# Kernel optimization log

Hardware: AMD Instinct MI355X
Metric: run time of the kernel (lower is better)

Reference implementation:

```python
import jax, jax.numpy as jnp
import numpy as np

R = 8          # n attention heads / input capsules (config_spin['r'])
U2 = 1024      # 2 * d_lstm
DA = 512       # d_a
SC = 128       # n_seen_class
OA = 16        # output_atoms
NR = 3         # n_routing
B = 128
T = 256


def setup_inputs() -> dict:
    key = jax.random.key(0)
    k1, k2, k3, k4 = jax.random.split(key, 4)
    x = jax.random.normal(k1, (B, T, U2), jnp.float32)              # encoder output outp
    WS1 = jax.random.normal(k2, (R, DA, U2), jnp.float32) * 0.03    # r stacked Linear(2u->d_a) weights
    WS2 = jax.random.normal(k3, (R, U2, DA), jnp.float32) * 0.03    # r stacked Linear(d_a->2u) weights
    capsule_weights = jax.random.normal(k4, (R, U2, SC * OA), jnp.float32) * 0.03
    return {"x": x, "WS1": WS1, "WS2": WS2, "capsule_weights": capsule_weights}


def _squash(s):
    # s: [B, out_dim, atoms]; squash along atoms (dim=2 in torch)
    norm = jnp.linalg.norm(s, axis=2, keepdims=True)
    n2 = norm * norm
    return s / norm * (n2 / (1.0 + n2))


def reference(x, WS1, WS2, capsule_weights):
    # --- encoder_dim_att: r-head structured self-attention ---
    hbar = jax.nn.relu(jnp.einsum('btu,rau->brta', x, WS1))          # [B,r,T,d_a]
    scores = jnp.einsum('brta,rua->brtu', hbar, WS2)                 # [B,r,T,2u]
    alphas = jax.nn.softmax(scores, axis=2)                          # softmax over seq (torch dim=1)
    m = jnp.einsum('brtu,btu->bru', alphas, x)                       # sentence_embedding [B,r,2u]

    # --- votes: tiled multiply+sum == contraction over input_atoms ---
    votes = jnp.einsum('bru,ruo->bro', m, capsule_weights)           # [B,r,SC*OA]
    votes = votes.reshape(B, R, SC, OA)                              # [B,r,SC,OA]

    # --- dynamic routing ---
    logits0 = jnp.zeros((B, R, SC), x.dtype)

    def step(logits, _):
        route = jax.nn.softmax(logits, axis=2)                       # [B,r,SC]
        preact = jnp.einsum('brc,brco->bco', route, votes)           # [B,SC,OA]
        act = _squash(preact)                                        # [B,SC,OA]
        dist = jnp.einsum('brco,bco->brc', votes, act)               # agreement [B,r,SC]
        return logits + dist, act

    _, acts = jax.lax.scan(step, logits0, None, length=NR)
    activation = acts[-1]                                            # last-iteration activation
    return jnp.linalg.norm(activation, axis=-1)                      # class logits [B,SC]
```

## Files before the change

### kernel.cpp

```cpp
#include <hip/hip_runtime.h>


typedef __attribute__((ext_vector_type(8))) short bf16x8;
typedef __attribute__((ext_vector_type(8))) unsigned short u16x8;
typedef __attribute__((ext_vector_type(4))) float f32x4;

#define LDT 40

__device__ __forceinline__ unsigned short f2bf(float f) {
    unsigned u = __float_as_uint(f);
    u += 0x7FFF + ((u >> 16) & 1);
    return (unsigned short)(u >> 16);
}
__device__ __forceinline__ float bf2f(unsigned short h) {
    return __uint_as_float(((unsigned)h) << 16);
}

typedef __attribute__((address_space(1))) void gvoid;
typedef __attribute__((address_space(3))) void lvoid;
__device__ __forceinline__ void gll16(const unsigned short* g, unsigned short* l) {
    __builtin_amdgcn_global_load_lds((gvoid*)g, (lvoid*)l, 16, 0, 0);
}

__global__ __launch_bounds__(256) void k0_hi(const float* __restrict__ src,
                                             unsigned short* __restrict__ hi,
                                             int n4) {
    int i = blockIdx.x * 256 + threadIdx.x;
    if (i >= n4) return;
    float4 v = ((const float4*)src)[i];
    ushort4 h;
    h.x = f2bf(v.x); h.y = f2bf(v.y); h.z = f2bf(v.z); h.w = f2bf(v.w);
    ((ushort4*)hi)[i] = h;
}

__global__ __launch_bounds__(256) void k0_tsplit(const float* __restrict__ cw,
                                                 unsigned short* __restrict__ ch,
                                                 unsigned short* __restrict__ cl) {
    __shared__ unsigned short Th[64 * 68], Tl[64 * 68];
    const int tid = threadIdx.x;
    const int n0 = blockIdx.x * 64, k0 = blockIdx.y * 64, r = blockIdx.z;
    const float* src = cw + (size_t)r * 1024 * 2048;
#pragma unroll
    for (int p = 0; p < 4; p++) {
        const int kl = p * 16 + (tid >> 4);
        const int nl = (tid & 15) * 4;
        float4 v = *(const float4*)(src + (size_t)(k0 + kl) * 2048 + n0 + nl);
        float vv[4] = {v.x, v.y, v.z, v.w};
#pragma unroll
        for (int e = 0; e < 4; e++) {
            unsigned short h = f2bf(vv[e]);
            Th[(nl + e) * 68 + kl] = h;
            Tl[(nl + e) * 68 + kl] = f2bf(vv[e] - bf2f(h));
        }
    }
    __syncthreads();
    const int nl = tid >> 2, kl = (tid & 3) * 16;
    unsigned short* dh = ch + ((size_t)r * 2048 + n0 + nl) * 1024 + k0 + kl;
    unsigned short* dl = cl + ((size_t)r * 2048 + n0 + nl) * 1024 + k0 + kl;
    *(u16x8*)(dh)     = *(const u16x8*)&Th[nl * 68 + kl];
    *(u16x8*)(dh + 8) = *(const u16x8*)&Th[nl * 68 + kl + 8];
    *(u16x8*)(dl)     = *(const u16x8*)&Tl[nl * 68 + kl];
    *(u16x8*)(dl + 8) = *(const u16x8*)&Tl[nl * 68 + kl + 8];
}

__global__ __launch_bounds__(256) void k1_hbar_gll(
    const unsigned short* __restrict__ Xb,
    const unsigned short* __restrict__ Wh,
    unsigned short* __restrict__ Hh) {
    __shared__ __align__(16) unsigned short Ah[128 * 32];
    __shared__ __align__(16) unsigned short Bh[128 * 32];
    const int tid = threadIdx.x;
    const int m0 = blockIdx.x * 128, n0 = blockIdx.y * 128;
    const int wave = tid >> 6, lane = tid & 63;
    const int wm = (wave >> 1) * 64, wn = (wave & 1) * 64;
    const int lx = lane & 15, qd = lane >> 4;
    const int rl = lane >> 2, cl = (lane & 3) * 8;

    f32x4 acc[4][4];
#pragma unroll
    for (int i = 0; i < 4; i++)
#pragma unroll
        for (int j = 0; j < 4; j++) acc[i][j] = (f32x4){0.f, 0.f, 0.f, 0.f};

    const unsigned short* asrc = Xb + (size_t)(m0 + rl) * 1024 + cl;
    const unsigned short* bsrc = Wh + (size_t)(n0 + rl) * 1024 + cl;

    for (int k0 = 0; k0 < 1024; k0 += 32) {
#pragma unroll
        for (int s = 0; s < 2; s++) {
            const int c = wave * 2 + s;
            gll16(asrc + (size_t)c * 16 * 1024 + k0, &Ah[c * 512]);
            gll16(bsrc + (size_t)c * 16 * 1024 + k0, &Bh[c * 512]);
        }
        __syncthreads();
        bf16x8 fa[4], fb[4];
#pragma unroll
        for (int i = 0; i < 4; i++) {
            fa[i] = *(const bf16x8*)&Ah[(wm + 16 * i + lx) * 32 + 8 * qd];
            fb[i] = *(const bf16x8*)&Bh[(wn + 16 * i + lx) * 32 + 8 * qd];
        }
#pragma unroll
        for (int i = 0; i < 4; i++)
#pragma unroll
            for (int j = 0; j < 4; j++)
                acc[i][j] = __builtin_amdgcn_mfma_f32_16x16x32_bf16(fa[i], fb[j], acc[i][j], 0, 0, 0);
        __syncthreads();
    }

#pragma unroll
    for (int i = 0; i < 4; i++)
#pragma unroll
        for (int j = 0; j < 4; j++) {
            const int col = n0 + wn + 16 * j + lx;
#pragma unroll
            for (int p = 0; p < 4; p++) {
                const int row = m0 + wm + 16 * i + 4 * qd + p;
                Hh[(size_t)row * 512 + col] = f2bf(fmaxf(acc[i][j][p], 0.f));
            }
        }
}

template <int XBF>
__global__ __launch_bounds__(256) void k1_hbar_mfma(
    const void* __restrict__ Xv,
    const unsigned short* __restrict__ Wh,
    unsigned short* __restrict__ Hh) {
    __shared__ unsigned short Ah[128 * LDT];
    __shared__ unsigned short Bh[128 * LDT];
    const int tid = threadIdx.x;
    const int m0 = blockIdx.x * 128, n0 = blockIdx.y * 128;
    const int wave = tid >> 6, lane = tid & 63;
    const int wm = (wave >> 1) * 64, wn = (wave & 1) * 64;
    const int lx = lane & 15, qd = lane >> 4;
    const int srow = tid >> 1, scol = (tid & 1) * 16;

    f32x4 acc[4][4];
#pragma unroll
    for (int i = 0; i < 4; i++)
#pragma unroll
        for (int j = 0; j < 4; j++) acc[i][j] = (f32x4){0.f, 0.f, 0.f, 0.f};

    const unsigned short* whrow = Wh + (size_t)(n0 + srow) * 1024 + scol;
    unsigned short* ah = &Ah[srow * LDT + scol];
    unsigned short* bh = &Bh[srow * LDT + scol];

    for (int k0 = 0; k0 < 1024; k0 += 32) {
        if (XBF) {
            const unsigned short* xrow =
                (const unsigned short*)Xv + (size_t)(m0 + srow) * 1024 + scol;
            u16x8 a0 = *(const u16x8*)(xrow + k0);
            u16x8 a1 = *(const u16x8*)(xrow + k0 + 8);
            *(u16x8*)(ah) = a0; *(u16x8*)(ah + 8) = a1;
        } else {
            const float* xrow = (const float*)Xv + (size_t)(m0 + srow) * 1024 + scol;
            float4 v0 = *(const float4*)(xrow + k0);
            float4 v1 = *(const float4*)(xrow + k0 + 4);
            float4 v2 = *(const float4*)(xrow + k0 + 8);
            float4 v3 = *(const float4*)(xrow + k0 + 12);
            float vv[16] = {v0.x, v0.y, v0.z, v0.w, v1.x, v1.y, v1.z, v1.w,
                            v2.x, v2.y, v2.z, v2.w, v3.x, v3.y, v3.z, v3.w};
            u16x8 p0, p1;
#pragma unroll
            for (int e = 0; e < 8; e++) p0[e] = f2bf(vv[e]);
#pragma unroll
            for (int e = 0; e < 8; e++) p1[e] = f2bf(vv[8 + e]);
            *(u16x8*)(ah) = p0; *(u16x8*)(ah + 8) = p1;
        }
        u16x8 b0 = *(const u16x8*)(whrow + k0);
        u16x8 b1 = *(const u16x8*)(whrow + k0 + 8);
        *(u16x8*)(bh) = b0; *(u16x8*)(bh + 8) = b1;
        __syncthreads();

        bf16x8 fa[4], fb[4];
#pragma unroll
        for (int i = 0; i < 4; i++) {
            fa[i] = *(const bf16x8*)&Ah[(wm + 16 * i + lx) * LDT + 8 * qd];
            fb[i] = *(const bf16x8*)&Bh[(wn + 16 * i + lx) * LDT + 8 * qd];
        }
#pragma unroll
        for (int i = 0; i < 4; i++)
#pragma unroll
            for (int j = 0; j < 4; j++)
                acc[i][j] = __builtin_amdgcn_mfma_f32_16x16x32_bf16(fa[i], fb[j], acc[i][j], 0, 0, 0);
        __syncthreads();
    }

#pragma unroll
    for (int i = 0; i < 4; i++)
#pragma unroll
        for (int j = 0; j < 4; j++) {
            const int col = n0 + wn + 16 * j + lx;
#pragma unroll
            for (int p = 0; p < 4; p++) {
                const int row = m0 + wm + 16 * i + 4 * qd + p;
                Hh[(size_t)row * 512 + col] = f2bf(fmaxf(acc[i][j][p], 0.f));
            }
        }
}

__global__ __launch_bounds__(256) void k2_mfma(
    const unsigned short* __restrict__ Hh,
    const unsigned short* __restrict__ W2h,
    const float* __restrict__ x, float* __restrict__ m_out, int b0, int r) {
    __shared__ __align__(16) unsigned short Ah[256 * 32];
    __shared__ __align__(16) unsigned short Bh[64 * 32];
    __shared__ float mred[256], sred[256], pred[256];
    const int tid = threadIdx.x;
    const int b_local = blockIdx.x, b = b0 + b_local;
    const int u0 = blockIdx.y * 64;
    const int wave = tid >> 6, lane = tid & 63;
    const int lx = lane & 15, qd = lane >> 4;
    const int rl = lane >> 2, cl = (lane & 3) * 8;

    f32x4 acc[4][4];
#pragma unroll
    for (int i = 0; i < 4; i++)
#pragma unroll
        for (int j = 0; j < 4; j++) acc[i][j] = (f32x4){0.f, 0.f, 0.f, 0.f};

    const unsigned short* asrc = Hh + (size_t)(b_local * 256 + rl) * 512 + cl;
    const int ub = wave * 16 + rl;
    const unsigned short* bsrc =
        W2h + (size_t)(u0 + 4 * (ub & 15) + (ub >> 4)) * 512 + cl;

    for (int k0 = 0; k0 < 512; k0 += 32) {
#pragma unroll
        for (int s = 0; s < 4; s++) {
            const int c = wave * 4 + s;
            gll16(asrc + (size_t)c * 16 * 512 + k0, &Ah[c * 512]);
        }
        gll16(bsrc + k0, &Bh[wave * 512]);
        __syncthreads();
        bf16x8 fa[4], fb[4];
#pragma unroll
        for (int i = 0; i < 4; i++) {
            fa[i] = *(const bf16x8*)&Ah[(64 * wave + 16 * i + lx) * 32 + 8 * qd];
            fb[i] = *(const bf16x8*)&Bh[(16 * i + lx) * 32 + 8 * qd];
        }
#pragma unroll
        for (int i = 0; i < 4; i++)
#pragma unroll
            for (int j = 0; j < 4; j++)
                acc[i][j] = __builtin_amdgcn_mfma_f32_16x16x32_bf16(fa[i], fb[j], acc[i][j], 0, 0, 0);
        __syncthreads();
    }

    float cm[4];
#pragma unroll
    for (int j = 0; j < 4; j++) {
        float mx = acc[0][j][0];
#pragma unroll
        for (int i = 0; i < 4; i++)
#pragma unroll
            for (int p = 0; p < 4; p++) mx = fmaxf(mx, acc[i][j][p]);
        mx = fmaxf(mx, __shfl_xor(mx, 16, 64));
        mx = fmaxf(mx, __shfl_xor(mx, 32, 64));
        if (qd == 0) mred[wave * 64 + 16 * j + lx] = mx;
    }
    __syncthreads();
#pragma unroll
    for (int j = 0; j < 4; j++) {
        const int c = 16 * j + lx;
        cm[j] = fmaxf(fmaxf(mred[c], mred[64 + c]), fmaxf(mred[128 + c], mred[192 + c]));
    }

    float ds[4] = {0.f, 0.f, 0.f, 0.f}, pm[4] = {0.f, 0.f, 0.f, 0.f};
    const float* xb = x + (size_t)b * 256 * 1024 + u0 + 4 * lx;
#pragma unroll
    for (int i = 0; i < 4; i++) {
#pragma unroll
        for (int p = 0; p < 4; p++) {
            const int t = 64 * wave + 16 * i + 4 * qd + p;
            float4 xv = *(const float4*)(xb + (size_t)t * 1024);
            float xa[4] = {xv.x, xv.y, xv.z, xv.w};
#pragma unroll
            for (int j = 0; j < 4; j++) {
                float e = __expf(acc[i][j][p] - cm[j]);
                ds[j] += e;
                pm[j] += e * xa[j];
            }
        }
    }
#pragma unroll
    for (int j = 0; j < 4; j++) {
        ds[j] += __shfl_xor(ds[j], 16, 64);
        ds[j] += __shfl_xor(ds[j], 32, 64);
        pm[j] += __shfl_xor(pm[j], 16, 64);
        pm[j] += __shfl_xor(pm[j], 32, 64);
        if (qd == 0) {
            sred[wave * 64 + 16 * j + lx] = ds[j];
            pred[wave * 64 + 16 * j + lx] = pm[j];
        }
    }
    __syncthreads();
    if (tid < 64) {
        float dsum = sred[tid] + sred[64 + tid] + sred[128 + tid] + sred[192 + tid];
        float psum = pred[tid] + pred[64 + tid] + pred[128 + tid] + pred[192 + tid];
        const int u = u0 + 4 * (tid & 15) + (tid >> 4);
        m_out[(size_t)(r * 128 + b) * 1024 + u] = psum / dsum;
    }
}

__global__ __launch_bounds__(256) void k3_votes_mfma(
    const float* __restrict__ Mb,
    const unsigned short* __restrict__ CWh,
    const unsigned short* __restrict__ CWl,
    float* __restrict__ V) {
    __shared__ unsigned short Ah[128 * LDT];
    __shared__ unsigned short Bh[64 * LDT], Bl[64 * LDT];
    const int tid = threadIdx.x;
    const int r = blockIdx.x, n0 = blockIdx.y * 64;
    const int wave = tid >> 6, lane = tid & 63;
    const int wr = wave >> 1, wc = wave & 1;
    const int lx = lane & 15, qd = lane >> 4;
    const int srow = tid >> 1, scol = (tid & 1) * 16;
    const int brow = tid >> 2, bcol = (tid & 3) * 8;

    const float* arow = Mb + (size_t)(r * 128 + srow) * 1024 + scol;
    const unsigned short* bhrow = CWh + ((size_t)r * 2048 + n0 + brow) * 1024 + bcol;
    const unsigned short* blrow = CWl + ((size_t)r * 2048 + n0 + brow) * 1024 + bcol;

    f32x4 acc[4][2];
#pragma unroll
    for (int i = 0; i < 4; i++)
#pragma unroll
        for (int j = 0; j < 2; j++) acc[i][j] = (f32x4){0.f, 0.f, 0.f, 0.f};

    for (int k0 = 0; k0 < 1024; k0 += 32) {
        float4 v0 = *(const float4*)(arow + k0);
        float4 v1 = *(const float4*)(arow + k0 + 4);
        float4 v2 = *(const float4*)(arow + k0 + 8);
        float4 v3 = *(const float4*)(arow + k0 + 12);
        float vv[16] = {v0.x, v0.y, v0.z, v0.w, v1.x, v1.y, v1.z, v1.w,
                        v2.x, v2.y, v2.z, v2.w, v3.x, v3.y, v3.z, v3.w};
        u16x8 p0, p1;
#pragma unroll
        for (int e = 0; e < 8; e++) p0[e] = f2bf(vv[e]);
#pragma unroll
        for (int e = 0; e < 8; e++) p1[e] = f2bf(vv[8 + e]);
        *(u16x8*)&Ah[srow * LDT + scol] = p0;
        *(u16x8*)&Ah[srow * LDT + scol + 8] = p1;
        *(u16x8*)&Bh[brow * LDT + bcol] = *(const u16x8*)(bhrow + k0);
        *(u16x8*)&Bl[brow * LDT + bcol] = *(const u16x8*)(blrow + k0);
        __syncthreads();

        bf16x8 fa[4], fbh[2], fbl[2];
#pragma unroll
        for (int i = 0; i < 4; i++)
            fa[i] = *(const bf16x8*)&Ah[(64 * wr + 16 * i + lx) * LDT + 8 * qd];
#pragma unroll
        for (int j = 0; j < 2; j++) {
            fbh[j] = *(const bf16x8*)&Bh[(32 * wc + 16 * j + lx) * LDT + 8 * qd];
            fbl[j] = *(const bf16x8*)&Bl[(32 * wc + 16 * j + lx) * LDT + 8 * qd];
        }
#pragma unroll
        for (int i = 0; i < 4; i++)
#pragma unroll
            for (int j = 0; j < 2; j++)
                acc[i][j] = __builtin_amdgcn_mfma_f32_16x16x32_bf16(fa[i], fbh[j], acc[i][j], 0, 0, 0);
#pragma unroll
        for (int i = 0; i < 4; i++)
#pragma unroll
            for (int j = 0; j < 2; j++)
                acc[i][j] = __builtin_amdgcn_mfma_f32_16x16x32_bf16(fa[i], fbl[j], acc[i][j], 0, 0, 0);
        __syncthreads();
    }

#pragma unroll
    for (int i = 0; i < 4; i++)
#pragma unroll
        for (int j = 0; j < 2; j++) {
            const int col = n0 + 32 * wc + 16 * j + lx;
#pragma unroll
            for (int p = 0; p < 4; p++) {
                const int row = 64 * wr + 16 * i + 4 * qd + p;
                V[((size_t)r * 128 + row) * 2048 + col] = acc[i][j][p];
            }
        }
}

__global__ __launch_bounds__(256) void k3_votes(const float* __restrict__ Mb,
                                                const float* __restrict__ CW,
                                                float* __restrict__ V) {
    __shared__ float As[16][132];
    __shared__ float Bs[16][132];
    const int tid = threadIdx.x;
    const int r = blockIdx.z;
    const int n0 = blockIdx.x * 128;
    const float* A = Mb + (size_t)r * 128 * 1024;
    const float* Bm = CW + (size_t)r * 1024 * 2048;
    float* C = V + (size_t)r * 128 * 2048;
    const int ty = tid >> 4, tx = tid & 15;
    const int k4 = (tid & 3) * 4, row = tid >> 2;
    const int n4 = (tid & 31) * 4, krow = tid >> 5;

    float acc[8][8];
#pragma unroll
    for (int i = 0; i < 8; i++)
#pragma unroll
        for (int j = 0; j < 8; j++) acc[i][j] = 0.f;

    for (int k0 = 0; k0 < 1024; k0 += 16) {
#pragma unroll
        for (int rr = 0; rr < 2; rr++) {
            const int m = row + rr * 64;
            float4 av = *(const float4*)(A + (size_t)m * 1024 + k0 + k4);
            As[k4 + 0][m] = av.x; As[k4 + 1][m] = av.y;
            As[k4 + 2][m] = av.z; As[k4 + 3][m] = av.w;
            const int k = krow + rr * 8;
            float4 bv = *(const float4*)(Bm + (size_t)(k0 + k) * 2048 + n0 + n4);
            *(float4*)(&Bs[k][n4]) = bv;
        }
        __syncthreads();
#pragma unroll
        for (int k = 0; k < 16; k++) {
            float a[8], b[8];
            *(float4*)(a)     = *(const float4*)(&As[k][ty * 8]);
            *(float4*)(a + 4) = *(const float4*)(&As[k][ty * 8 + 4]);
            *(float4*)(b)     = *(const float4*)(&Bs[k][tx * 8]);
            *(float4*)(b + 4) = *(const float4*)(&Bs[k][tx * 8 + 4]);
#pragma unroll
            for (int i = 0; i < 8; i++)
#pragma unroll
                for (int j = 0; j < 8; j++) acc[i][j] += a[i] * b[j];
        }
        __syncthreads();
    }
#pragma unroll
    for (int i = 0; i < 8; i++) {
        const int m = ty * 8 + i;
#pragma unroll
        for (int j = 0; j < 8; j += 4) {
            float4 v;
            v.x = acc[i][j + 0]; v.y = acc[i][j + 1];
            v.z = acc[i][j + 2]; v.w = acc[i][j + 3];
            *(float4*)(C + (size_t)m * 2048 + n0 + tx * 8 + j) = v;
        }
    }
}

__global__ __launch_bounds__(256) void k4_routing(const float* __restrict__ V,
                                                  float* __restrict__ out) {
    __shared__ float logits[8 * 128];
    __shared__ float route[8 * 128];
    __shared__ float preact[128 * 16];
    __shared__ float act[128 * 16];
    __shared__ float fred[128];
    const int b = blockIdx.x, tid = threadIdx.x;
    const float* vb = V + (size_t)b * 2048;

    for (int i = tid; i < 1024; i += 256) logits[i] = 0.f;
    __syncthreads();

    for (int it = 0; it < 3; it++) {
        {
            const int r = tid >> 5, g = tid & 31;
            float l[4];
#pragma unroll
            for (int q = 0; q < 4; q++) l[q] = logits[r * 128 + g + q * 32];
            float mx = fmaxf(fmaxf(l[0], l[1]), fmaxf(l[2], l[3]));
            for (int msk = 16; msk; msk >>= 1) mx = fmaxf(mx, __shfl_xor(mx, msk, 32));
            float e[4], s = 0.f;
#pragma unroll
            for (int q = 0; q < 4; q++) { e[q] = expf(l[q] - mx); s += e[q]; }
            for (int msk = 16; msk; msk >>= 1) s += __shfl_xor(s, msk, 32);
            float inv = 1.f / s;
#pragma unroll
            for (int q = 0; q < 4; q++) route[r * 128 + g + q * 32] = e[q] * inv;
        }
        __syncthreads();
        for (int i = tid; i < 2048; i += 256) {
            const int c = i >> 4;
            float a = 0.f;
#pragma unroll
            for (int r = 0; r < 8; r++)
                a += route[r * 128 + c] * vb[(size_t)r * 128 * 2048 + i];
            preact[i] = a;
        }
        __syncthreads();
        if (tid < 128) {
            float n2 = 0.f;
#pragma unroll
            for (int o = 0; o < 16; o++) { float p = preact[tid * 16 + o]; n2 += p * p; }
            fred[tid] = sqrtf(n2) / (1.f + n2);
        }
        __syncthreads();
        for (int i = tid; i < 2048; i += 256) act[i] = preact[i] * fred[i >> 4];
        __syncthreads();
        for (int i = tid; i < 1024; i += 256) {
            const int r = i >> 7, c = i & 127;
            float d = 0.f;
#pragma unroll
            for (int o = 0; o < 16; o++)
                d += vb[(size_t)r * 128 * 2048 + c * 16 + o] * act[c * 16 + o];
            logits[i] += d;
        }
        __syncthreads();
    }
    if (tid < 128) {
        float n2 = 0.f;
#pragma unroll
        for (int o = 0; o < 16; o++) { float a = act[tid * 16 + o]; n2 += a * a; }
        out[(size_t)b * 128 + tid] = sqrtf(n2);
    }
}

extern "C" void kernel_launch(void* const* d_in, const int* in_sizes, int n_in,
                              void* d_out, int out_size, void* d_ws, size_t ws_size,
                              hipStream_t stream) {
    const float* x   = (const float*)d_in[0];
    const float* WS1 = (const float*)d_in[1];
    const float* WS2 = (const float*)d_in[2];
    const float* cw  = (const float*)d_in[3];
    float* out = (float*)d_out;

    char* ws = (char*)d_ws;
    float* m_buf = (float*)ws;
    float* votes = (float*)(ws + ((size_t)4 << 20));
    unsigned short* W1h = (unsigned short*)(ws + ((size_t)12 << 20));
    unsigned short* W2h = (unsigned short*)(ws + ((size_t)20 << 20));

    const bool use_cw  = ws_size >= ((size_t)124 << 20);
    const bool use_xbf = ws_size >= ((size_t)188 << 20);
    unsigned short* CWh = (unsigned short*)(ws + ((size_t)28 << 20));
    unsigned short* CWl = (unsigned short*)(ws + ((size_t)60 << 20));
    unsigned short* Xbf = (unsigned short*)(ws + ((size_t)92 << 20));
    const size_t hh_off = use_xbf ? ((size_t)156 << 20)
                        : use_cw  ? ((size_t)92 << 20)
                                  : ((size_t)28 << 20);
    unsigned short* Hh = (unsigned short*)(ws + hh_off);

    int CB = 128;
    {
        const size_t perb = (size_t)256 << 10;
        if (ws_size < hh_off + 128 * perb) {
            size_t avail = (ws_size > hh_off) ? (ws_size - hh_off) : perb;
            CB = (int)(avail / perb);
            if (CB < 1) CB = 1;
            if (CB > 128) CB = 128;
        }
    }

    const int nW4 = (8 * 512 * 1024) / 4;
    k0_hi<<<dim3((nW4 + 255) / 256), dim3(256), 0, stream>>>(WS1, W1h, nW4);
    k0_hi<<<dim3((nW4 + 255) / 256), dim3(256), 0, stream>>>(WS2, W2h, nW4);
    if (use_cw)
        k0_tsplit<<<dim3(32, 16, 8), dim3(256), 0, stream>>>(cw, CWh, CWl);
    if (use_xbf) {
        const int nX4 = (128 * 256 * 1024) / 4;
        k0_hi<<<dim3((nX4 + 255) / 256), dim3(256), 0, stream>>>(x, Xbf, nX4);
    }

    for (int b0 = 0; b0 < 128; b0 += CB) {
        const int bc = (128 - b0 < CB) ? (128 - b0) : CB;
        for (int r = 0; r < 8; r++) {
            if (use_xbf)
                k1_hbar_gll<<<dim3(bc * 2, 4), dim3(256), 0, stream>>>(
                    Xbf + (size_t)b0 * 256 * 1024,
                    W1h + (size_t)r * 512 * 1024, Hh);
            else
                k1_hbar_mfma<0><<<dim3(bc * 2, 4), dim3(256), 0, stream>>>(
                    (const void*)(x + (size_t)b0 * 256 * 1024),
                    W1h + (size_t)r * 512 * 1024, Hh);
            k2_mfma<<<dim3(bc, 16), dim3(256), 0, stream>>>(
                Hh, W2h + (size_t)r * 1024 * 512, x, m_buf, b0, r);
        }
    }
    if (use_cw)
        k3_votes_mfma<<<dim3(8, 32), dim3(256), 0, stream>>>(m_buf, CWh, CWl, votes);
    else
        k3_votes<<<dim3(16, 1, 8), dim3(256), 0, stream>>>(m_buf, cw, votes);
    k4_routing<<<dim3(128), dim3(256), 0, stream>>>(votes, out);
}
```

Baseline: 1.487 ms.

## Batch all heads per launch and double-buffer LDS loads in hbar/score GEMMs

Replaces the per-head k1/k2 launch loop with kernels that cover all 8 heads per launch, processing 32-batch chunks, so there are far fewer launches and larger grids. Both GEMMs now double-buffer the LDS tiles, issuing the next global_load_lds before computing on the current tile, to overlap memory with MFMA. The workspace is re-laid out, with CW split buffers aliasing the Hh region after the main loop. This adds more LDS per block, which may lower occupancy.

```diff
diff --git a/kernel.cpp b/kernel.cpp
--- a/kernel.cpp
+++ b/kernel.cpp
@@ -63,14 +63,14 @@
     *(u16x8*)(dl + 8) = *(const u16x8*)&Tl[nl * 68 + kl + 8];
 }
 
-__global__ __launch_bounds__(256) void k1_hbar_gll(
+__global__ __launch_bounds__(256) void k1_all(
     const unsigned short* __restrict__ Xb,
-    const unsigned short* __restrict__ Wh,
-    unsigned short* __restrict__ Hh) {
-    __shared__ __align__(16) unsigned short Ah[128 * 32];
-    __shared__ __align__(16) unsigned short Bh[128 * 32];
+    const unsigned short* __restrict__ W1h,
+    unsigned short* __restrict__ HhA) {
+    __shared__ __align__(16) unsigned short Ah[2][128 * 32];
+    __shared__ __align__(16) unsigned short Bh[2][128 * 32];
     const int tid = threadIdx.x;
-    const int m0 = blockIdx.x * 128, n0 = blockIdx.y * 128;
+    const int m0 = blockIdx.x * 128, n0 = blockIdx.y * 128, r = blockIdx.z;
     const int wave = tid >> 6, lane = tid & 63;
     const int wm = (wave >> 1) * 64, wn = (wave & 1) * 64;
     const int lx = lane & 15, qd = lane >> 4;
@@ -83,21 +83,30 @@
         for (int j = 0; j < 4; j++) acc[i][j] = (f32x4){0.f, 0.f, 0.f, 0.f};
 
     const unsigned short* asrc = Xb + (size_t)(m0 + rl) * 1024 + cl;
-    const unsigned short* bsrc = Wh + (size_t)(n0 + rl) * 1024 + cl;
-
-    for (int k0 = 0; k0 < 1024; k0 += 32) {
-#pragma unroll
-        for (int s = 0; s < 2; s++) {
-            const int c = wave * 2 + s;
-            gll16(asrc + (size_t)c * 16 * 1024 + k0, &Ah[c * 512]);
-            gll16(bsrc + (size_t)c * 16 * 1024 + k0, &Bh[c * 512]);
-        }
-        __syncthreads();
+    const unsigned short* bsrc =
+        W1h + (size_t)r * 512 * 1024 + (size_t)(n0 + rl) * 1024 + cl;
+
+#define K1_STAGE(AD, BD, KK)                                         \
+    do {                                                             \
+        _Pragma("unroll") for (int s = 0; s < 2; s++) {              \
+            const int c = wave * 2 + s;                              \
+            gll16(asrc + (size_t)c * 16 * 1024 + (KK), (AD) + c * 512); \
+            gll16(bsrc + (size_t)c * 16 * 1024 + (KK), (BD) + c * 512); \
+        }                                                            \
+    } while (0)
+
+    K1_STAGE(Ah[0], Bh[0], 0);
+    __syncthreads();
+    int p = 0;
+    for (int t = 0; t < 32; ++t) {
+        if (t < 31) K1_STAGE(Ah[p ^ 1], Bh[p ^ 1], (t + 1) * 32);
+        const unsigned short* Ab = Ah[p];
+        const unsigned short* Bb = Bh[p];
         bf16x8 fa[4], fb[4];
 #pragma unroll
         for (int i = 0; i < 4; i++) {
-            fa[i] = *(const bf16x8*)&Ah[(wm + 16 * i + lx) * 32 + 8 * qd];
-            fb[i] = *(const bf16x8*)&Bh[(wn + 16 * i + lx) * 32 + 8 * qd];
+            fa[i] = *(const bf16x8*)&Ab[(wm + 16 * i + lx) * 32 + 8 * qd];
+            fb[i] = *(const bf16x8*)&Bb[(wn + 16 * i + lx) * 32 + 8 * qd];
         }
 #pragma unroll
         for (int i = 0; i < 4; i++)
@@ -105,17 +114,20 @@
             for (int j = 0; j < 4; j++)
                 acc[i][j] = __builtin_amdgcn_mfma_f32_16x16x32_bf16(fa[i], fb[j], acc[i][j], 0, 0, 0);
         __syncthreads();
-    }
-
+        p ^= 1;
+    }
+#undef K1_STAGE
+
+    unsigned short* Hh = HhA + (size_t)r * 8192 * 512;
 #pragma unroll
     for (int i = 0; i < 4; i++)
 #pragma unroll
         for (int j = 0; j < 4; j++) {
             const int col = n0 + wn + 16 * j + lx;
 #pragma unroll
-            for (int p = 0; p < 4; p++) {
-                const int row = m0 + wm + 16 * i + 4 * qd + p;
-                Hh[(size_t)row * 512 + col] = f2bf(fmaxf(acc[i][j][p], 0.f));
+            for (int p2 = 0; p2 < 4; p2++) {
+                const int row = m0 + wm + 16 * i + 4 * qd + p2;
+                Hh[(size_t)row * 512 + col] = f2bf(fmaxf(acc[i][j][p2], 0.f));
             }
         }
 }
@@ -198,6 +210,127 @@
         }
 }
 
+__global__ __launch_bounds__(256) void k2_allr(
+    const unsigned short* __restrict__ HhA,
+    const unsigned short* __restrict__ W2h,
+    const float* __restrict__ x, float* __restrict__ m_out, int b0) {
+    __shared__ __align__(16) unsigned short Ah[2][256 * 32];
+    __shared__ __align__(16) unsigned short Bh[2][64 * 32];
+    __shared__ float mred[256], sred[256], pred[256];
+    const int tid = threadIdx.x;
+    const int b_local = blockIdx.x, b = b0 + b_local;
+    const int u0 = blockIdx.y * 64;
+    const int r_base = blockIdx.z * 4;
+    const int wave = tid >> 6, lane = tid & 63;
+    const int lx = lane & 15, qd = lane >> 4;
+    const int rl = lane >> 2, cl = (lane & 3) * 8;
+    const int ub = wave * 16 + rl;
+    const int uperm = 4 * (ub & 15) + (ub >> 4);
+
+    for (int rr = 0; rr < 4; ++rr) {
+        const int r = r_base + rr;
+        const unsigned short* asrc =
+            HhA + (size_t)r * 8192 * 512 + (size_t)(b_local * 256 + rl) * 512 + cl;
+        const unsigned short* bsrc =
+            W2h + (size_t)r * 1024 * 512 + (size_t)(u0 + uperm) * 512 + cl;
+
+        f32x4 acc[4][4];
+#pragma unroll
+        for (int i = 0; i < 4; i++)
+#pragma unroll
+            for (int j = 0; j < 4; j++) acc[i][j] = (f32x4){0.f, 0.f, 0.f, 0.f};
+
+#define K2_STAGE(AD, BD, KK)                                            \
+    do {                                                                \
+        _Pragma("unroll") for (int s = 0; s < 4; s++) {                 \
+            const int c = wave * 4 + s;                                 \
+            gll16(asrc + (size_t)c * 16 * 512 + (KK), (AD) + c * 512);  \
+        }                                                               \
+        gll16(bsrc + (KK), (BD) + wave * 512);                          \
+    } while (0)
+
+        K2_STAGE(Ah[0], Bh[0], 0);
+        __syncthreads();
+        int p = 0;
+        for (int t = 0; t < 16; ++t) {
+            if (t < 15) K2_STAGE(Ah[p ^ 1], Bh[p ^ 1], (t + 1) * 32);
+            const unsigned short* Ab = Ah[p];
+            const unsigned short* Bb = Bh[p];
+            bf16x8 fa[4], fb[4];
+#pragma unroll
+            for (int i = 0; i < 4; i++) {
+                fa[i] = *(const bf16x8*)&Ab[(64 * wave + 16 * i + lx) * 32 + 8 * qd];
+                fb[i] = *(const bf16x8*)&Bb[(16 * i + lx) * 32 + 8 * qd];
+            }
+#pragma unroll
+            for (int i = 0; i < 4; i++)
+#pragma unroll
+                for (int j = 0; j < 4; j++)
+                    acc[i][j] = __builtin_amdgcn_mfma_f32_16x16x32_bf16(fa[i], fb[j], acc[i][j], 0, 0, 0);
+            __syncthreads();
+            p ^= 1;
+        }
+#undef K2_STAGE
+
+        float cm[4];
+#pragma unroll
+        for (int j = 0; j < 4; j++) {
+            float mx = acc[0][j][0];
+#pragma unroll
+            for (int i = 0; i < 4; i++)
+#pragma unroll
+                for (int p2 = 0; p2 < 4; p2++) mx = fmaxf(mx, acc[i][j][p2]);
+            mx = fmaxf(mx, __shfl_xor(mx, 16, 64));
+            mx = fmaxf(mx, __shfl_xor(mx, 32, 64));
+            if (qd == 0) mred[wave * 64 + 16 * j + lx] = mx;
+        }
+        __syncthreads();
+#pragma unroll
+        for (int j = 0; j < 4; j++) {
+            const int c = 16 * j + lx;
+            cm[j] = fmaxf(fmaxf(mred[c], mred[64 + c]),
+                          fmaxf(mred[128 + c], mred[192 + c]));
+        }
+
+        float ds[4] = {0.f, 0.f, 0.f, 0.f}, pm[4] = {0.f, 0.f, 0.f, 0.f};
+        const float* xb = x + (size_t)b * 256 * 1024 + u0 + 4 * lx;
+#pragma unroll
+        for (int i = 0; i < 4; i++) {
+#pragma unroll
+            for (int p2 = 0; p2 < 4; p2++) {
+                const int t = 64 * wave + 16 * i + 4 * qd + p2;
+                float4 xv = *(const float4*)(xb + (size_t)t * 1024);
+                float xa[4] = {xv.x, xv.y, xv.z, xv.w};
+#pragma unroll
+                for (int j = 0; j < 4; j++) {
+                    float e = __expf(acc[i][j][p2] - cm[j]);
+                    ds[j] += e;
+                    pm[j] += e * xa[j];
+                }
+            }
+        }
+#pragma unroll
+        for (int j = 0; j < 4; j++) {
+            ds[j] += __shfl_xor(ds[j], 16, 64);
+            ds[j] += __shfl_xor(ds[j], 32, 64);
+            pm[j] += __shfl_xor(pm[j], 16, 64);
+            pm[j] += __shfl_xor(pm[j], 32, 64);
+            if (qd == 0) {
+                sred[wave * 64 + 16 * j + lx] = ds[j];
+                pred[wave * 64 + 16 * j + lx] = pm[j];
+            }
+        }
+        __syncthreads();
+        if (tid < 64) {
+            float dsum = sred[tid] + sred[64 + tid] + sred[128 + tid] + sred[192 + tid];
+            float psum = pred[tid] + pred[64 + tid] + pred[128 + tid] + pred[192 + tid];
+            const int u = u0 + 4 * (tid & 15) + (tid >> 4);
+            m_out[(size_t)(r * 128 + b) * 1024 + u] = psum / dsum;
+        }
+        __syncthreads();
+    }
+}
+
 __global__ __launch_bounds__(256) void k2_mfma(
     const unsigned short* __restrict__ Hh,
     const unsigned short* __restrict__ W2h,
@@ -522,53 +655,62 @@
 
     const bool use_cw  = ws_size >= ((size_t)124 << 20);
     const bool use_xbf = ws_size >= ((size_t)188 << 20);
-    unsigned short* CWh = (unsigned short*)(ws + ((size_t)28 << 20));
-    unsigned short* CWl = (unsigned short*)(ws + ((size_t)60 << 20));
-    unsigned short* Xbf = (unsigned short*)(ws + ((size_t)92 << 20));
-    const size_t hh_off = use_xbf ? ((size_t)156 << 20)
-                        : use_cw  ? ((size_t)92 << 20)
-                                  : ((size_t)28 << 20);
-    unsigned short* Hh = (unsigned short*)(ws + hh_off);
-
-    int CB = 128;
-    {
-        const size_t perb = (size_t)256 << 10;
-        if (ws_size < hh_off + 128 * perb) {
-            size_t avail = (ws_size > hh_off) ? (ws_size - hh_off) : perb;
-            CB = (int)(avail / perb);
-            if (CB < 1) CB = 1;
-            if (CB > 128) CB = 128;
-        }
-    }
 
     const int nW4 = (8 * 512 * 1024) / 4;
     k0_hi<<<dim3((nW4 + 255) / 256), dim3(256), 0, stream>>>(WS1, W1h, nW4);
     k0_hi<<<dim3((nW4 + 255) / 256), dim3(256), 0, stream>>>(WS2, W2h, nW4);
-    if (use_cw)
-        k0_tsplit<<<dim3(32, 16, 8), dim3(256), 0, stream>>>(cw, CWh, CWl);
+
     if (use_xbf) {
+        unsigned short* Xbf = (unsigned short*)(ws + ((size_t)28 << 20));
+        unsigned short* HhA = (unsigned short*)(ws + ((size_t)92 << 20));
+        unsigned short* CWh = (unsigned short*)(ws + ((size_t)92 << 20));
+        unsigned short* CWl = (unsigned short*)(ws + ((size_t)124 << 20));
+
         const int nX4 = (128 * 256 * 1024) / 4;
         k0_hi<<<dim3((nX4 + 255) / 256), dim3(256), 0, stream>>>(x, Xbf, nX4);
-    }
-
-    for (int b0 = 0; b0 < 128; b0 += CB) {
-        const int bc = (128 - b0 < CB) ? (128 - b0) : CB;
-        for (int r = 0; r < 8; r++) {
-            if (use_xbf)
-                k1_hbar_gll<<<dim3(bc * 2, 4), dim3(256), 0, stream>>>(
-                    Xbf + (size_t)b0 * 256 * 1024,
-                    W1h + (size_t)r * 512 * 1024, Hh);
-            else
+
+        for (int b0 = 0; b0 < 128; b0 += 32) {
+            k1_all<<<dim3(64, 4, 8), dim3(256), 0, stream>>>(
+                Xbf + (size_t)b0 * 256 * 1024, W1h, HhA);
+            k2_allr<<<dim3(32, 16, 2), dim3(256), 0, stream>>>(
+                HhA, W2h, x, m_buf, b0);
+        }
+        k0_tsplit<<<dim3(32, 16, 8), dim3(256), 0, stream>>>(cw, CWh, CWl);
+        k3_votes_mfma<<<dim3(8, 32), dim3(256), 0, stream>>>(m_buf, CWh, CWl, votes);
+    } else {
+        unsigned short* CWh = (unsigned short*)(ws + ((size_t)28 << 20));
+        unsigned short* CWl = (unsigned short*)(ws + ((size_t)60 << 20));
+        const size_t hh_off = use_cw ? ((size_t)92 << 20) : ((size_t)28 << 20);
+        unsigned short* Hh = (unsigned short*)(ws + hh_off);
+
+        int CB = 128;
+        {
+            const size_t perb = (size_t)256 << 10;
+            if (ws_size < hh_off + 128 * perb) {
+                size_t avail = (ws_size > hh_off) ? (ws_size - hh_off) : perb;
+                CB = (int)(avail / perb);
+                if (CB < 1) CB = 1;
+                if (CB > 128) CB = 128;
+            }
+        }
+
+        if (use_cw)
+            k0_tsplit<<<dim3(32, 16, 8), dim3(256), 0, stream>>>(cw, CWh, CWl);
+
+        for (int b0 = 0; b0 < 128; b0 += CB) {
+            const int bc = (128 - b0 < CB) ? (128 - b0) : CB;
+            for (int r = 0; r < 8; r++) {
                 k1_hbar_mfma<0><<<dim3(bc * 2, 4), dim3(256), 0, stream>>>(
                     (const void*)(x + (size_t)b0 * 256 * 1024),
                     W1h + (size_t)r * 512 * 1024, Hh);
-            k2_mfma<<<dim3(bc, 16), dim3(256), 0, stream>>>(
-                Hh, W2h + (size_t)r * 1024 * 512, x, m_buf, b0, r);
-        }
-    }
-    if (use_cw)
-        k3_votes_mfma<<<dim3(8, 32), dim3(256), 0, stream>>>(m_buf, CWh, CWl, votes);
-    else
-        k3_votes<<<dim3(16, 1, 8), dim3(256), 0, stream>>>(m_buf, cw, votes);
+                k2_mfma<<<dim3(bc, 16), dim3(256), 0, stream>>>(
+                    Hh, W2h + (size_t)r * 1024 * 512, x, m_buf, b0, r);
+            }
+        }
+        if (use_cw)
+            k3_votes_mfma<<<dim3(8, 32), dim3(256), 0, stream>>>(m_buf, CWh, CWl, votes);
+        else
+            k3_votes<<<dim3(16, 1, 8), dim3(256), 0, stream>>>(m_buf, cw, votes);
+    }
     k4_routing<<<dim3(128), dim3(256), 0, stream>>>(votes, out);
 }
```

After: 1.233 ms. 1.21x faster.
